# Kernel optimization log

Hardware: AMD Instinct MI355X
Metric: run time of the kernel (lower is better)

The kernel has to match this reference:

```python
import jax, jax.numpy as jnp
import numpy as np

B, S, T = 512, 512, 128


def setup_inputs() -> dict:
    key = jax.random.key(0)
    k1, k2, k3, k4, k5 = jax.random.split(key, 5)
    emissions = jax.random.normal(k1, (B, S, T), dtype=jnp.float32)
    tags = jax.random.randint(k2, (B, S), 0, T, dtype=jnp.int32)
    mask = jnp.ones((B, S), dtype=jnp.int32)
    start_transitions = jax.random.uniform(k3, (T,), minval=-0.1, maxval=0.1, dtype=jnp.float32)
    end_transitions = jax.random.uniform(k4, (T,), minval=-0.1, maxval=0.1, dtype=jnp.float32)
    transitions = jax.random.uniform(k5, (T, T), minval=-0.1, maxval=0.1, dtype=jnp.float32)
    return {"emissions": emissions, "tags": tags, "mask": mask,
            "start_transitions": start_transitions,
            "end_transitions": end_transitions,
            "transitions": transitions}


def reference(emissions, tags, mask, start_transitions, end_transitions, transitions):
    b, s, t = emissions.shape
    maskf = mask.astype(emissions.dtype)
    barange = jnp.arange(b)

    # ---- numerator: score of the gold path (vectorized over timesteps) ----
    score = start_transitions[tags[:, 0]] + emissions[barange, 0, tags[:, 0]]
    # transition scores tags[i-1] -> tags[i], shape (B, S-1)
    trans_steps = transitions[tags[:, :-1], tags[:, 1:]]
    # emission score of gold tag at each step, shape (B, S)
    em_steps = jnp.take_along_axis(emissions, tags[:, :, None], axis=2)[:, :, 0]
    score = score + jnp.sum((trans_steps + em_steps[:, 1:]) * maskf[:, 1:], axis=1)
    seq_ends = mask.astype(jnp.int32).sum(axis=1) - 1
    last_tags = tags[barange, seq_ends]
    score = score + end_transitions[last_tags]

    # ---- denominator: log partition via forward recurrence (lax.scan) ----
    init = start_transitions[None, :] + emissions[:, 0, :]  # (B, T)

    def step(scores, inp):
        em_i, m_i = inp  # (B, T), (B,)
        # (B, T_prev, T_next) semiring matmul in log-space
        nxt = jax.nn.logsumexp(
            scores[:, :, None] + transitions[None, :, :] + em_i[:, None, :], axis=1)
        scores = jnp.where(m_i[:, None] > 0, nxt, scores)
        return scores, None

    ems = jnp.moveaxis(emissions[:, 1:, :], 1, 0)  # (S-1, B, T)
    ms = jnp.moveaxis(mask[:, 1:], 1, 0)           # (S-1, B)
    final, _ = jax.lax.scan(step, init, (ems, ms))
    denom = jax.nn.logsumexp(final + end_transitions[None, :], axis=1)  # (B,)

    return jnp.sum(score - denom)
```

## Files before the change

### kernel.cpp

```cpp
#include <hip/hip_runtime.h>
#include <math.h>


#define T 128
#define SLEN 512
#define BATCH 512

__global__ __launch_bounds__(512, 2)
__attribute__((amdgpu_waves_per_eu(2, 2)))
void fwd_kernel(
    const float* __restrict__ em, const int* __restrict__ tags,
    const int* __restrict__ mask, const float* __restrict__ startT,
    const float* __restrict__ endT, const float* __restrict__ trans,
    float* __restrict__ ws)
{
    const int tid = threadIdx.x;
    const int h   = tid >> 8;
    const int u   = tid & 255;
    const int rg  = u & 7;
    const int cg  = u >> 3;
    const int q   = rg & 3;
    const int b   = 2 * blockIdx.x + h;
    const int jc  = 4 * cg + q;
    const float* emb = em + (size_t)b * SLEN * T;
    const int*   mk  = mask + (size_t)b * SLEN;

    int craw[4], slot[4];
#pragma unroll
    for (int i = 0; i < 4; ++i) {
        craw[i] = 4 * rg + ((i + rg) & 3);
        slot[i] = craw[i] ^ ((craw[i] & 16) ? 4 : 0);
    }

    float4 Ef[4][4];
#pragma unroll
    for (int i = 0; i < 4; ++i) {
        const int r0 = 4 * craw[i];
#pragma unroll
        for (int qq = 0; qq < 4; ++qq) {
            const int col = 4 * cg + qq;
            Ef[i][qq].x = __expf(trans[(r0 + 0) * T + col]);
            Ef[i][qq].y = __expf(trans[(r0 + 1) * T + col]);
            Ef[i][qq].z = __expf(trans[(r0 + 2) * T + col]);
            Ef[i][qq].w = __expf(trans[(r0 + 3) * T + col]);
        }
    }

    __shared__ __align__(16) float4 psh[2][2][32];
    __shared__ float sig_sh[2][2];
    __shared__ float redm[8], reds[8], redn[8];
    __shared__ int   redc[8];

    const char* rp[4];
#pragma unroll
    for (int i = 0; i < 4; ++i)
        rp[i] = (const char*)&psh[h][0][0] + slot[i] * 16;
    const int scg = cg ^ ((cg & 16) ? 4 : 0);
    char* wp = (char*)&psh[h][0][0] + scg * 16 + q * 4;

    float score = startT[jc] + emb[jc];
    if (rg < 4) *(float*)(wp + 512) = __expf(score);
    if (u == 0) sig_sh[h][1] = score;
    float sigma = 0.f;

    float emv[4], emn[4];
    int   mkv[4], mkn[4];
#pragma unroll
    for (int k = 0; k < 4; ++k) { emv[k] = (emb + (1 + k) * T)[jc]; mkv[k] = mk[1 + k]; }
    __syncthreads();

    const bool lb0 = (rg & 1) != 0, lb1 = (rg & 2) != 0;

    for (int s0 = 1; s0 < SLEN; s0 += 4) {
#pragma unroll
        for (int k = 0; k < 4; ++k) {
            int ss = s0 + 4 + k; ss = (ss < SLEN) ? ss : (SLEN - 1);
            emn[k] = (emb + ss * T)[jc];
            mkn[k] = mk[ss];
        }
#pragma unroll
        for (int k = 0; k < 4; ++k) {
            const int s = s0 + k;
            if (s < SLEN) {
                const int cur = (1 + k) & 1;
                float a0 = 0.f, a1 = 0.f, a2 = 0.f, a3 = 0.f;
#pragma unroll
                for (int i = 0; i < 4; ++i) {
                    const float4 pv = *(const float4*)(rp[i] + cur * 512);
                    a0 = fmaf(pv.x, Ef[i][0].x, a0); a0 = fmaf(pv.y, Ef[i][0].y, a0);
                    a0 = fmaf(pv.z, Ef[i][0].z, a0); a0 = fmaf(pv.w, Ef[i][0].w, a0);
                    a1 = fmaf(pv.x, Ef[i][1].x, a1); a1 = fmaf(pv.y, Ef[i][1].y, a1);
                    a1 = fmaf(pv.z, Ef[i][1].z, a1); a1 = fmaf(pv.w, Ef[i][1].w, a1);
                    a2 = fmaf(pv.x, Ef[i][2].x, a2); a2 = fmaf(pv.y, Ef[i][2].y, a2);
                    a2 = fmaf(pv.z, Ef[i][2].z, a2); a2 = fmaf(pv.w, Ef[i][2].w, a2);
                    a3 = fmaf(pv.x, Ef[i][3].x, a3); a3 = fmaf(pv.y, Ef[i][3].y, a3);
                    a3 = fmaf(pv.z, Ef[i][3].z, a3); a3 = fmaf(pv.w, Ef[i][3].w, a3);
                }
                float P  = (lb0 ? a1 : a0) + __shfl_xor(lb0 ? a0 : a1, 1);
                float P2 = (lb0 ? a3 : a2) + __shfl_xor(lb0 ? a2 : a3, 1);
                float t  = (lb1 ? P2 : P) + __shfl_xor(lb1 ? P : P2, 2);
                t += __shfl_xor(t, 4);
                const float sig_next = sig_sh[h][cur];
                const float n = sigma + __logf(t) + emv[k];
                score = (mkv[k] > 0) ? n : score;
                const float pp = __expf(score - sig_next);
                if (rg < 4) *(float*)(wp + (cur ^ 1) * 512) = pp;
                if (u == 0) sig_sh[h][cur ^ 1] = score;
                sigma = sig_next;
                __syncthreads();
            }
        }
#pragma unroll
        for (int k = 0; k < 4; ++k) { emv[k] = emn[k]; mkv[k] = mkn[k]; }
    }

    const int wid = tid >> 6;
    float v = score + endT[jc];
    float m = v;
#pragma unroll
    for (int off = 32; off; off >>= 1) m = fmaxf(m, __shfl_xor(m, off));
    if ((tid & 63) == 0) redm[wid] = m;
    __syncthreads();
    float M = redm[4 * h];
#pragma unroll
    for (int i = 1; i < 4; ++i) M = fmaxf(M, redm[4 * h + i]);
    float sm = __expf(v - M) * 0.5f;
#pragma unroll
    for (int off = 32; off; off >>= 1) sm += __shfl_xor(sm, off);
    if ((tid & 63) == 0) reds[wid] = sm;

    const int* tg = tags + (size_t)b * SLEN;
    float nv = 0.f; int cnt = 0;
#pragma unroll
    for (int rep = 0; rep < 2; ++rep) {
        const int s = u + 256 * rep;
        const int mm = mk[s];
        cnt += (mm != 0);
        if (s >= 1 && mm > 0)
            nv += trans[tg[s - 1] * T + tg[s]] + emb[s * T + tg[s]];
    }
#pragma unroll
    for (int off = 32; off; off >>= 1) {
        nv  += __shfl_xor(nv, off);
        cnt += __shfl_xor(cnt, off);
    }
    if ((tid & 63) == 0) { redn[wid] = nv; redc[wid] = cnt; }
    __syncthreads();
    if (u == 0) {
        float ssum = 0.f, nsum = 0.f; int seqlen = 0;
#pragma unroll
        for (int i = 0; i < 4; ++i) {
            ssum += reds[4 * h + i]; nsum += redn[4 * h + i]; seqlen += redc[4 * h + i];
        }
        const float denom = M + __logf(ssum);
        const int t0 = tg[0], tl = tg[seqlen - 1];
        ws[b] = (startT[t0] + emb[t0] + endT[tl] + nsum) - denom;
    }
}

__global__ __launch_bounds__(256) void reduce_kernel(
    const float* __restrict__ ws, float* __restrict__ out)
{
    const int t = threadIdx.x;
    float local = 0.f;
    for (int i = t; i < BATCH; i += 256) local += ws[i];
    __shared__ float rf[256];
    rf[t] = local;
    __syncthreads();
    for (int off = 128; off > 0; off >>= 1) {
        if (t < off) rf[t] += rf[t + off];
        __syncthreads();
    }
    if (t == 0) out[0] = rf[0];
}

extern "C" void kernel_launch(void* const* d_in, const int* in_sizes, int n_in,
                              void* d_out, int out_size, void* d_ws, size_t ws_size,
                              hipStream_t stream)
{
    const float* emissions = (const float*)d_in[0];
    const int*   tags      = (const int*)d_in[1];
    const int*   mask      = (const int*)d_in[2];
    const float* startT    = (const float*)d_in[3];
    const float* endT      = (const float*)d_in[4];
    const float* trans     = (const float*)d_in[5];
    float* out = (float*)d_out;
    float* ws  = (float*)d_ws;

    fwd_kernel<<<BATCH / 2, 512, 0, stream>>>(emissions, tags, mask, startT, endT, trans, ws);
    reduce_kernel<<<1, 256, 0, stream>>>(ws, out);
}
```

Before: 399.2 us.

## Use one batch row per 256-thread block and packed v2f FMAs

Each block now handles a single sequence with 256 threads, where before one 512-thread block processed two sequences, and the grid doubles to match. This means each per-step __syncthreads only couples 4 waves instead of 8, and the waves_per_eu attribute is dropped. The inner semiring dot product is rewritten with 2-wide vector FMAs so the compiler can emit packed FP32 FMA instructions, followed by one extra horizontal add per accumulator. The risk is a different occupancy and scheduling profile with more blocks.

```diff
diff --git a/kernel.cpp b/kernel.cpp
--- a/kernel.cpp
+++ b/kernel.cpp
@@ -6,21 +6,19 @@
 #define SLEN 512
 #define BATCH 512
 
-__global__ __launch_bounds__(512, 2)
-__attribute__((amdgpu_waves_per_eu(2, 2)))
-void fwd_kernel(
+typedef float v2f __attribute__((ext_vector_type(2)));
+
+__global__ __launch_bounds__(256, 2) void fwd_kernel(
     const float* __restrict__ em, const int* __restrict__ tags,
     const int* __restrict__ mask, const float* __restrict__ startT,
     const float* __restrict__ endT, const float* __restrict__ trans,
     float* __restrict__ ws)
 {
     const int tid = threadIdx.x;
-    const int h   = tid >> 8;
-    const int u   = tid & 255;
-    const int rg  = u & 7;
-    const int cg  = u >> 3;
+    const int rg  = tid & 7;
+    const int cg  = tid >> 3;
     const int q   = rg & 3;
-    const int b   = 2 * blockIdx.x + h;
+    const int b   = blockIdx.x;
     const int jc  = 4 * cg + q;
     const float* emb = em + (size_t)b * SLEN * T;
     const int*   mk  = mask + (size_t)b * SLEN;
@@ -32,35 +30,35 @@
         slot[i] = craw[i] ^ ((craw[i] & 16) ? 4 : 0);
     }
 
-    float4 Ef[4][4];
+    v2f Elo[4][4], Ehi[4][4];
 #pragma unroll
     for (int i = 0; i < 4; ++i) {
         const int r0 = 4 * craw[i];
 #pragma unroll
         for (int qq = 0; qq < 4; ++qq) {
             const int col = 4 * cg + qq;
-            Ef[i][qq].x = __expf(trans[(r0 + 0) * T + col]);
-            Ef[i][qq].y = __expf(trans[(r0 + 1) * T + col]);
-            Ef[i][qq].z = __expf(trans[(r0 + 2) * T + col]);
-            Ef[i][qq].w = __expf(trans[(r0 + 3) * T + col]);
+            Elo[i][qq] = (v2f){ __expf(trans[(r0 + 0) * T + col]),
+                                __expf(trans[(r0 + 1) * T + col]) };
+            Ehi[i][qq] = (v2f){ __expf(trans[(r0 + 2) * T + col]),
+                                __expf(trans[(r0 + 3) * T + col]) };
         }
     }
 
-    __shared__ __align__(16) float4 psh[2][2][32];
-    __shared__ float sig_sh[2][2];
-    __shared__ float redm[8], reds[8], redn[8];
-    __shared__ int   redc[8];
+    __shared__ __align__(16) float4 psh[2][32];
+    __shared__ float sig_sh[2];
+    __shared__ float redm[4], reds[4], redn[4];
+    __shared__ int   redc[4];
 
     const char* rp[4];
 #pragma unroll
     for (int i = 0; i < 4; ++i)
-        rp[i] = (const char*)&psh[h][0][0] + slot[i] * 16;
+        rp[i] = (const char*)&psh[0][0] + slot[i] * 16;
     const int scg = cg ^ ((cg & 16) ? 4 : 0);
-    char* wp = (char*)&psh[h][0][0] + scg * 16 + q * 4;
+    char* wp = (char*)&psh[0][0] + scg * 16 + q * 4;
 
     float score = startT[jc] + emb[jc];
     if (rg < 4) *(float*)(wp + 512) = __expf(score);
-    if (u == 0) sig_sh[h][1] = score;
+    if (tid == 0) sig_sh[1] = score;
     float sigma = 0.f;
 
     float emv[4], emn[4];
@@ -83,29 +81,32 @@
             const int s = s0 + k;
             if (s < SLEN) {
                 const int cur = (1 + k) & 1;
-                float a0 = 0.f, a1 = 0.f, a2 = 0.f, a3 = 0.f;
+                v2f a0 = {0.f, 0.f}, a1 = a0, a2 = a0, a3 = a0;
 #pragma unroll
                 for (int i = 0; i < 4; ++i) {
                     const float4 pv = *(const float4*)(rp[i] + cur * 512);
-                    a0 = fmaf(pv.x, Ef[i][0].x, a0); a0 = fmaf(pv.y, Ef[i][0].y, a0);
-                    a0 = fmaf(pv.z, Ef[i][0].z, a0); a0 = fmaf(pv.w, Ef[i][0].w, a0);
-                    a1 = fmaf(pv.x, Ef[i][1].x, a1); a1 = fmaf(pv.y, Ef[i][1].y, a1);
-                    a1 = fmaf(pv.z, Ef[i][1].z, a1); a1 = fmaf(pv.w, Ef[i][1].w, a1);
-                    a2 = fmaf(pv.x, Ef[i][2].x, a2); a2 = fmaf(pv.y, Ef[i][2].y, a2);
-                    a2 = fmaf(pv.z, Ef[i][2].z, a2); a2 = fmaf(pv.w, Ef[i][2].w, a2);
-                    a3 = fmaf(pv.x, Ef[i][3].x, a3); a3 = fmaf(pv.y, Ef[i][3].y, a3);
-                    a3 = fmaf(pv.z, Ef[i][3].z, a3); a3 = fmaf(pv.w, Ef[i][3].w, a3);
+                    const v2f plo = {pv.x, pv.y}, phi = {pv.z, pv.w};
+                    a0 = __builtin_elementwise_fma(plo, Elo[i][0], a0);
+                    a0 = __builtin_elementwise_fma(phi, Ehi[i][0], a0);
+                    a1 = __builtin_elementwise_fma(plo, Elo[i][1], a1);
+                    a1 = __builtin_elementwise_fma(phi, Ehi[i][1], a1);
+                    a2 = __builtin_elementwise_fma(plo, Elo[i][2], a2);
+                    a2 = __builtin_elementwise_fma(phi, Ehi[i][2], a2);
+                    a3 = __builtin_elementwise_fma(plo, Elo[i][3], a3);
+                    a3 = __builtin_elementwise_fma(phi, Ehi[i][3], a3);
                 }
-                float P  = (lb0 ? a1 : a0) + __shfl_xor(lb0 ? a0 : a1, 1);
-                float P2 = (lb0 ? a3 : a2) + __shfl_xor(lb0 ? a2 : a3, 1);
+                const float c0 = a0.x + a0.y, c1 = a1.x + a1.y;
+                const float c2 = a2.x + a2.y, c3 = a3.x + a3.y;
+                float P  = (lb0 ? c1 : c0) + __shfl_xor(lb0 ? c0 : c1, 1);
+                float P2 = (lb0 ? c3 : c2) + __shfl_xor(lb0 ? c2 : c3, 1);
                 float t  = (lb1 ? P2 : P) + __shfl_xor(lb1 ? P : P2, 2);
                 t += __shfl_xor(t, 4);
-                const float sig_next = sig_sh[h][cur];
+                const float sig_next = sig_sh[cur];
                 const float n = sigma + __logf(t) + emv[k];
                 score = (mkv[k] > 0) ? n : score;
                 const float pp = __expf(score - sig_next);
                 if (rg < 4) *(float*)(wp + (cur ^ 1) * 512) = pp;
-                if (u == 0) sig_sh[h][cur ^ 1] = score;
+                if (tid == 0) sig_sh[cur ^ 1] = score;
                 sigma = sig_next;
                 __syncthreads();
             }
@@ -121,9 +122,9 @@
     for (int off = 32; off; off >>= 1) m = fmaxf(m, __shfl_xor(m, off));
     if ((tid & 63) == 0) redm[wid] = m;
     __syncthreads();
-    float M = redm[4 * h];
+    float M = redm[0];
 #pragma unroll
-    for (int i = 1; i < 4; ++i) M = fmaxf(M, redm[4 * h + i]);
+    for (int i = 1; i < 4; ++i) M = fmaxf(M, redm[i]);
     float sm = __expf(v - M) * 0.5f;
 #pragma unroll
     for (int off = 32; off; off >>= 1) sm += __shfl_xor(sm, off);
@@ -133,7 +134,7 @@
     float nv = 0.f; int cnt = 0;
 #pragma unroll
     for (int rep = 0; rep < 2; ++rep) {
-        const int s = u + 256 * rep;
+        const int s = tid + 256 * rep;
         const int mm = mk[s];
         cnt += (mm != 0);
         if (s >= 1 && mm > 0)
@@ -146,11 +147,11 @@
     }
     if ((tid & 63) == 0) { redn[wid] = nv; redc[wid] = cnt; }
     __syncthreads();
-    if (u == 0) {
+    if (tid == 0) {
         float ssum = 0.f, nsum = 0.f; int seqlen = 0;
 #pragma unroll
         for (int i = 0; i < 4; ++i) {
-            ssum += reds[4 * h + i]; nsum += redn[4 * h + i]; seqlen += redc[4 * h + i];
+            ssum += reds[i]; nsum += redn[i]; seqlen += redc[i];
         }
         const float denom = M + __logf(ssum);
         const int t0 = tg[0], tl = tg[seqlen - 1];
@@ -187,6 +188,6 @@
     float* out = (float*)d_out;
     float* ws  = (float*)d_ws;
 
-    fwd_kernel<<<BATCH / 2, 512, 0, stream>>>(emissions, tags, mask, startT, endT, trans, ws);
+    fwd_kernel<<<BATCH, 256, 0, stream>>>(emissions, tags, mask, startT, endT, trans, ws);
     reduce_kernel<<<1, 256, 0, stream>>>(ws, out);
 }
```

After: 398.0 us. No clear change (-0.3%).
